# Performance work log

Hardware: AMD Instinct MI355X
Metric: run time of the kernel (lower is better)

Reference implementation:

```python
import jax, jax.numpy as jnp
import numpy as np

D_MODEL, D_STATE, L = 512, 64, 1024
BATCH = 8


def setup_inputs() -> dict:
    key = jax.random.key(0)
    ks = jax.random.split(key, 8)
    dt_min, dt_max = 1e-3, 1e-1
    log_dt = jax.random.uniform(ks[0], (D_MODEL,)) * (np.log(dt_max) - np.log(dt_min)) + np.log(dt_min)
    log_A_real = jnp.log(0.5 * jnp.ones((D_MODEL, D_STATE)))
    A_imag = jnp.pi * jnp.tile(jnp.arange(D_STATE, dtype=jnp.float32), (D_MODEL, 1))
    B_real = jnp.ones((D_MODEL, D_STATE), jnp.float32)
    B_imag = jnp.zeros((D_MODEL, D_STATE), jnp.float32)
    C_real = jax.random.normal(ks[1], (D_MODEL, D_STATE))
    C_imag = jax.random.normal(ks[2], (D_MODEL, D_STATE))
    D = jax.random.normal(ks[3], (D_MODEL,))
    # 1x1 conv (Conv1d kernel_size=1) -> weight (2H, H), bias (2H,)
    conv_w = jax.random.normal(ks[4], (2 * D_MODEL, D_MODEL)) / np.sqrt(D_MODEL)
    conv_b = jnp.zeros((2 * D_MODEL,), jnp.float32)
    dec_w = jax.random.normal(ks[5], (1, D_MODEL)) / np.sqrt(D_MODEL)
    dec_b = jnp.zeros((1,), jnp.float32)
    u = jax.random.normal(ks[6], (BATCH, D_MODEL, L))
    return dict(u=u, log_dt=log_dt, log_A_real=log_A_real, A_imag=A_imag,
                B_real=B_real, B_imag=B_imag, C_real=C_real, C_imag=C_imag,
                D=D, conv_w=conv_w, conv_b=conv_b, dec_w=dec_w, dec_b=dec_b)


def _s4d_kernel(log_dt, log_A_real, A_imag, B_real, B_imag, C_real, C_imag, Lk):
    dt = jnp.exp(log_dt)                              # (H,)
    A = -jnp.exp(log_A_real) + 1j * A_imag            # (H, N) complex
    dtA = A * dt[:, None]                             # (H, N)
    A_bar = jnp.exp(dtA)
    Bc = B_real + 1j * B_imag
    B_bar = (A_bar - 1.0) / A * Bc                    # ZOH discretization
    Cc = C_real + 1j * C_imag
    t = jnp.arange(Lk)                                # (L,)
    # A_bar^t = exp(dtA * t); fuse C*B_bar weighting, reduce over state N
    A_pow = jnp.exp(dtA[:, :, None] * t)              # (H, N, L)
    K = jnp.einsum('hn,hnl->hl', Cc * B_bar, A_pow)   # (H, L) complex
    return K.real


def reference(u, log_dt, log_A_real, A_imag, B_real, B_imag, C_real, C_imag,
              D, conv_w, conv_b, dec_w, dec_b):
    H, Lk = u.shape[1], u.shape[2]
    K = _s4d_kernel(log_dt, log_A_real, A_imag, B_real, B_imag, C_real, C_imag, Lk)
    # depthwise cross-correlation (torch conv1d semantics), padding L-1, keep first L
    y = jax.lax.conv_general_dilated(
        u, K[:, None, :], window_strides=(1,), padding=[(Lk - 1, Lk - 1)],
        feature_group_count=H, dimension_numbers=('NCH', 'OIH', 'NCH'))
    y = y[:, :, :Lk]
    y = y + u * D[:, None]
    y = jax.nn.gelu(y, approximate=False)
    # 1x1 conv + GLU over channel dim
    z = jnp.einsum('oc,bcl->bol', conv_w, y) + conv_b[:, None]
    a, b = jnp.split(z, 2, axis=1)
    y = a * jax.nn.sigmoid(b)                         # (B, H, L)
    pooled = y.mean(axis=-1)                          # (B, H)
    return pooled @ dec_w.T + dec_b                   # (B, 1)
```

## Files before the change

### kernel.cpp

```cpp
#include <hip/hip_runtime.h>
#include <hip/hip_bf16.h>
#include <math.h>

typedef __attribute__((ext_vector_type(8))) short short8;
typedef __attribute__((ext_vector_type(4))) float f32x4;
typedef __attribute__((ext_vector_type(16))) float f32x16;
typedef __attribute__((ext_vector_type(4))) unsigned int uint4v;

constexpr int Hm = 512, Lm = 1024, Bm = 8;

static __device__ __forceinline__ unsigned short f2bf(float f) {
    __hip_bfloat16 h = __float2bfloat16(f);
    return *reinterpret_cast<unsigned short*>(&h);
}
static __device__ __forceinline__ float bf2f(unsigned short u) {
    return __uint_as_float((unsigned)u << 16);
}
static __device__ __forceinline__ uint2 pack4(const unsigned short* x) {
    return make_uint2((unsigned)x[0] | ((unsigned)x[1] << 16),
                      (unsigned)x[2] | ((unsigned)x[3] << 16));
}
static __device__ __forceinline__ short8 ld16u(const char* p) {
    uint2 a = *(const uint2*)p;
    uint2 b = *(const uint2*)(p + 8);
    uint4v t = { a.x, a.y, b.x, b.y };
    return __builtin_bit_cast(short8, t);
}

__global__ __launch_bounds__(256, 2) void k_tconv(const float* __restrict__ log_dt,
                                                  const float* __restrict__ log_A_real,
                                                  const float* __restrict__ A_imag,
                                                  const float* __restrict__ B_real,
                                                  const float* __restrict__ B_imag,
                                                  const float* __restrict__ C_real,
                                                  const float* __restrict__ C_imag,
                                                  const float* __restrict__ conv_w,
                                                  const float* __restrict__ u,
                                                  const float* __restrict__ Dvec,
                                                  unsigned short* __restrict__ Woh,
                                                  unsigned short* __restrict__ YbfH) {
    __shared__ __align__(16) char smem[41984];
    const int tid = threadIdx.x, lane = tid & 63, w = tid >> 6;
    const int h = blockIdx.x;
    const int m = lane & 31, q = lane >> 5;
    const int cg = (lane >> 3) & 3, b = lane & 7;
    float* Kf = (float*)(smem + 36352);
    float* pl = (float*)(smem + 40448);

    float4 ureg[8];
    {
        const int b2 = tid >> 5, t32 = tid & 31;
        const float* ub = u + ((size_t)(b2 * 512 + h)) * 1024;
        #pragma unroll
        for (int g = 0; g < 8; ++g) ureg[g] = *(const float4*)&ub[t32 * 4 + g * 128];
    }
    const float Dh = Dvec[h];

    {
        int i = h * 1024 + tid * 4;
        float4 v = *(const float4*)&conv_w[i];
        *(uint2*)&Woh[i] = make_uint2((unsigned)f2bf(v.x) | ((unsigned)f2bf(v.y) << 16),
                                      (unsigned)f2bf(v.z) | ((unsigned)f2bf(v.w) << 16));
    }
    if (tid < 64) {
        int idx = h * 64 + tid;
        double dt = exp((double)log_dt[h]);
        double Ar = -exp((double)log_A_real[idx]);
        double Ai = (double)A_imag[idx];
        double ar = Ar * dt, ai = Ai * dt;
        double er = exp(ar);
        double rr = er * cos(ai), ri = er * sin(ai);
        double nr = rr - 1.0, ni = ri;
        double den = Ar * Ar + Ai * Ai;
        double qr = (nr * Ar + ni * Ai) / den;
        double qi = (ni * Ar - nr * Ai) / den;
        double Br = (double)B_real[idx], Bi = (double)B_imag[idx];
        double bbr = qr * Br - qi * Bi, bbi = qr * Bi + qi * Br;
        double Cr = (double)C_real[idx], Ci = (double)C_imag[idx];
        double wr = Cr * bbr - Ci * bbi, wi = Cr * bbi + Ci * bbr;
        double e64 = exp(ar * 64.0);
        double p64 = ai * 64.0;
        pl[0 * 64 + tid] = (float)rr;
        pl[1 * 64 + tid] = (float)ri;
        pl[2 * 64 + tid] = (float)wr;
        pl[3 * 64 + tid] = (float)wi;
        pl[4 * 64 + tid] = (float)(e64 * cos(p64));
        pl[5 * 64 + tid] = (float)(e64 * sin(p64));
    }
    __syncthreads();

    {
        float* kl = (float*)(smem + 17792) + w * 1056;
        const float rrf = pl[0 * 64 + lane], rif = pl[1 * 64 + lane];
        float pr = pl[2 * 64 + lane], pi = pl[3 * 64 + lane];
        float br = pl[4 * 64 + lane], bi = pl[5 * 64 + lane];
        int cc = w * 4;
        while (cc) {
            if (cc & 1) { float t_ = pr * br - pi * bi; pi = fmaf(pr, bi, pi * br); pr = t_; }
            float t2 = br * br - bi * bi; bi = 2.f * br * bi; br = t2;
            cc >>= 1;
        }
        const int jj = lane & 15, nq = lane >> 4;
        for (int qq = 0; qq < 16; ++qq) {
            #pragma unroll
            for (int j = 0; j < 16; ++j) {
                kl[j * 66 + lane] = pr;
                float t_ = pr * rrf - pi * rif; pi = fmaf(pr, rif, pi * rrf); pr = t_;
            }
            asm volatile("s_waitcnt lgkmcnt(0)" ::: "memory");
            float s0 = 0.f, s1 = 0.f;
            #pragma unroll
            for (int n = 0; n < 16; n += 4) {
                float2 a = *(const float2*)&kl[jj * 66 + nq * 16 + n];
                float2 b2 = *(const float2*)&kl[jj * 66 + nq * 16 + n + 2];
                s0 += a.x + a.y; s1 += b2.x + b2.y;
            }
            float s = s0 + s1;
            s += __shfl_xor(s, 16);
            s += __shfl_xor(s, 32);
            if (lane < 16) Kf[w * 256 + qq * 16 + jj] = s;
            asm volatile("s_waitcnt lgkmcnt(0)" ::: "memory");
        }
    }
    __syncthreads();

    {
        unsigned int* Gd = (unsigned int*)smem;
        for (int t = tid; t < 4448; t += 256) {
            int s = t / 556;
            int d = t - s * 556;
            int idx0 = 2 * d + s;
            float k0 = (idx0 < 1024) ? Kf[idx0] : 0.f;
            float k1 = (idx0 + 1 < 1024) ? Kf[idx0 + 1] : 0.f;
            Gd[t] = (unsigned)f2bf(k0) | ((unsigned)f2bf(k1) << 16);
        }
    }
    if (tid < 8) { uint4 z = {0, 0, 0, 0}; ((uint4*)(smem + 36224))[tid] = z; }
    __syncthreads();

    {
        const int b2 = tid >> 5, t32 = tid & 31;
        #pragma unroll
        for (int g = 0; g < 8; ++g) {
            int s = t32 * 4 + g * 128;
            float4 v = ureg[g];
            unsigned short t0 = f2bf(v.x), t1 = f2bf(v.y), t2 = f2bf(v.z), t3 = f2bf(v.w);
            int jc = s >> 6, e = s & 63;
            *(uint2*)(smem + 17792 + jc * 1152 + b2 * 144 + e * 2) =
                make_uint2((unsigned)t0 | ((unsigned)t1 << 16),
                           (unsigned)t2 | ((unsigned)t3 << 16));
        }
    }
    __syncthreads();

    const int icg = (cg == 0) ? w : (cg == 1) ? 7 - w : (cg == 2) ? 8 + w : 15 - w;
    const int dmax = 15 - w;

    int aU = 17792 + icg * 1152 + b * 144 + q * 16;
    const int zl = 36224 + q * 16;

    const int sA = (7 - m) & 7;
    int baseH = sA * 2224 + (991 - m - sA + 8 * q) * 2;

    const f32x16 zacc = {};
    f32x16 acc0 = zacc, acc1 = zacc;

    short8 m2, m1, w0, w1, w2, w3;
#define LDA() { const char* pH = smem + baseH; \
        m2 = *(const short8*)(pH +   0); m1 = *(const short8*)(pH +  32); \
        w0 = *(const short8*)(pH +  64); w1 = *(const short8*)(pH +  96); \
        w2 = *(const short8*)(pH + 128); w3 = *(const short8*)(pH + 160); }
    LDA();

    for (int d = 0; d <= dmax; ++d) {
        const char* pb = smem + ((d <= icg) ? aU : zl);
        short8 b0 = *(const short8*)(pb +  0);
        short8 b1 = *(const short8*)(pb + 32);
        short8 b2 = *(const short8*)(pb + 64);
        short8 b3 = *(const short8*)(pb + 96);
        acc0 = __builtin_amdgcn_mfma_f32_32x32x16_bf16(w0, b0, acc0, 0, 0, 0);
        acc1 = __builtin_amdgcn_mfma_f32_32x32x16_bf16(m2, b0, acc1, 0, 0, 0);
        acc0 = __builtin_amdgcn_mfma_f32_32x32x16_bf16(w1, b1, acc0, 0, 0, 0);
        acc1 = __builtin_amdgcn_mfma_f32_32x32x16_bf16(m1, b1, acc1, 0, 0, 0);
        acc0 = __builtin_amdgcn_mfma_f32_32x32x16_bf16(w2, b2, acc0, 0, 0, 0);
        acc1 = __builtin_amdgcn_mfma_f32_32x32x16_bf16(w0, b2, acc1, 0, 0, 0);
        acc0 = __builtin_amdgcn_mfma_f32_32x32x16_bf16(w3, b3, acc0, 0, 0, 0);
        acc1 = __builtin_amdgcn_mfma_f32_32x32x16_bf16(w1, b3, acc1, 0, 0, 0);
        baseH -= 128; aU -= 1152;
        if (d < dmax) LDA();
    }
#undef LDA

    __syncthreads();

    #pragma unroll
    for (int mf = 0; mf < 2; ++mf) {
        const f32x16 ac = mf ? acc1 : acc0;
        #pragma unroll
        for (int rq = 0; rq < 4; ++rq) {
            const int row0 = mf * 32 + 8 * rq + 4 * q;
            uint2 uv2 = *(const uint2*)(smem + 17792 + icg * 1152 + b * 144 + row0 * 2);
            unsigned short us[4] = { (unsigned short)(uv2.x & 0xffff),
                                     (unsigned short)(uv2.x >> 16),
                                     (unsigned short)(uv2.y & 0xffff),
                                     (unsigned short)(uv2.y >> 16) };
            unsigned short oh[4];
            #pragma unroll
            for (int k = 0; k < 4; ++k) {
                float y = ac[rq * 4 + k] + Dh * bf2f(us[k]);
                float g = 0.5f * y * (1.0f + erff(y * 0.70710678118654752f));
                oh[k] = f2bf(g);
            }
            *(uint2*)(smem + icg * 1088 + b * 136 + row0 * 2) = pack4(oh);
        }
    }
    __syncthreads();
    {
        const int b2 = tid >> 5, t32 = tid & 31;
        unsigned short* dst = YbfH + ((size_t)(b2 * 512 + h)) * 1024;
        #pragma unroll
        for (int g = 0; g < 8; ++g) {
            int s = t32 * 4 + g * 128;
            int jc = s >> 6, e = s & 63;
            uint2 v = *(const uint2*)(smem + jc * 1088 + b2 * 136 + e * 2);
            *(uint2*)&dst[s] = v;
        }
    }
}

__global__ __launch_bounds__(256) void k2_gemm(const unsigned short* __restrict__ WbfH,
                                               const unsigned short* __restrict__ Ybf,
                                               const float* __restrict__ conv_b,
                                               const float* __restrict__ dec_w,
                                               float* __restrict__ partial) {
    __shared__ unsigned short WTh[128][40];
    __shared__ unsigned short YT[128][44];
    __shared__ float red[4][64][20];
    const int tid = threadIdx.x, lane = tid & 63, wid = tid >> 6;
    const int b = blockIdx.z, oblk = blockIdx.y, lblk = blockIdx.x;
    const int o0 = oblk * 64, l0 = lblk * 128;
    const int fr = lane & 15, fq = lane >> 4;

    f32x4 acc[8][2] = {};

    const int srow = tid >> 1, skh = (tid & 1) * 16;
    const int grow = (srow < 64) ? (o0 + srow) : (512 + o0 + srow - 64);
    const size_t woff = (size_t)grow * 512 + skh;
    const int cp = tid & 15, lg = tid >> 4;
    const unsigned short* ysb = Ybf + ((size_t)(b * 512 + 2 * cp)) * 1024 + l0 + lg * 8;

    uint4 wc0 = *(const uint4*)(WbfH + woff);
    uint4 wc1 = *(const uint4*)(WbfH + woff + 8);
    uint4 yc0 = *(const uint4*)(ysb);
    uint4 yc1 = *(const uint4*)(ysb + 1024);

    for (int c0 = 0; c0 < 512; c0 += 32) {
        __syncthreads();
        *(uint4*)&WTh[srow][skh]     = wc0;
        *(uint4*)&WTh[srow][skh + 8] = wc1;
        {
            const unsigned int* a = (const unsigned int*)&yc0;
            const unsigned int* c = (const unsigned int*)&yc1;
            #pragma unroll
            for (int t2 = 0; t2 < 4; ++t2) {
                unsigned int lo = (a[t2] & 0xffffu) | (c[t2] << 16);
                unsigned int hi = (a[t2] >> 16) | (c[t2] & 0xffff0000u);
                *(unsigned int*)&YT[lg * 8 + 2 * t2][2 * cp] = lo;
                *(unsigned int*)&YT[lg * 8 + 2 * t2 + 1][2 * cp] = hi;
            }
        }
        if (c0 + 32 < 512) {
            wc0 = *(const uint4*)(WbfH + woff + c0 + 32);
            wc1 = *(const uint4*)(WbfH + woff + c0 + 40);
            const unsigned short* ysn = ysb + (size_t)(c0 + 32) * 1024;
            yc0 = *(const uint4*)(ysn);
            yc1 = *(const uint4*)(ysn + 1024);
        }
        __syncthreads();
        short8 b0h = ld16u((const char*)&YT[wid * 32 + fr][fq * 8]);
        short8 b1h = ld16u((const char*)&YT[wid * 32 + 16 + fr][fq * 8]);
        #pragma unroll
        for (int mf = 0; mf < 8; ++mf) {
            short8 ah = *(const short8*)&WTh[mf * 16 + fr][fq * 8];
            acc[mf][0] = __builtin_amdgcn_mfma_f32_16x16x32_bf16(ah, b0h, acc[mf][0], 0, 0, 0);
            acc[mf][1] = __builtin_amdgcn_mfma_f32_16x16x32_bf16(ah, b1h, acc[mf][1], 0, 0, 0);
        }
    }

    #pragma unroll
    for (int mf = 0; mf < 4; ++mf)
        #pragma unroll
        for (int j = 0; j < 4; ++j) {
            int ol = mf * 16 + fq * 4 + j;
            float ba = conv_b[o0 + ol];
            float bb = conv_b[512 + o0 + ol];
            float s = 0.f;
            #pragma unroll
            for (int nf = 0; nf < 2; ++nf) {
                float za = acc[mf][nf][j] + ba;
                float zb = acc[mf + 4][nf][j] + bb;
                s += za / (1.f + expf(-zb));
            }
            red[wid][ol][fr] = s;
        }
    __syncthreads();
    if (tid < 64) {
        float s = 0.f;
        #pragma unroll
        for (int w = 0; w < 4; ++w) {
            float4 r0 = *(const float4*)&red[w][tid][0];
            float4 r1 = *(const float4*)&red[w][tid][4];
            float4 r2 = *(const float4*)&red[w][tid][8];
            float4 r3 = *(const float4*)&red[w][tid][12];
            s += (r0.x + r0.y + r0.z + r0.w) + (r1.x + r1.y + r1.z + r1.w)
               + (r2.x + r2.y + r2.z + r2.w) + (r3.x + r3.y + r3.z + r3.w);
        }
        float val = s * dec_w[o0 + tid] * (1.0f / 1024.0f);
        #pragma unroll
        for (int off = 32; off; off >>= 1) val += __shfl_xor(val, off);
        if (tid == 0) partial[((b * 8) + oblk) * 8 + lblk] = val;
    }
}

__global__ void k3_final(const float* __restrict__ partial,
                         const float* __restrict__ dec_b,
                         float* __restrict__ out) {
    int b = threadIdx.x;
    if (b < Bm) {
        float s = dec_b[0];
        for (int i = 0; i < 64; ++i) s += partial[b * 64 + i];
        out[b] = s;
    }
}

extern "C" void kernel_launch(void* const* d_in, const int* in_sizes, int n_in,
                              void* d_out, int out_size, void* d_ws, size_t ws_size,
                              hipStream_t stream) {
    const float* u          = (const float*)d_in[0];
    const float* log_dt     = (const float*)d_in[1];
    const float* log_A_real = (const float*)d_in[2];
    const float* A_imag     = (const float*)d_in[3];
    const float* B_real     = (const float*)d_in[4];
    const float* B_imag     = (const float*)d_in[5];
    const float* C_real     = (const float*)d_in[6];
    const float* C_imag     = (const float*)d_in[7];
    const float* Dvec       = (const float*)d_in[8];
    const float* conv_w     = (const float*)d_in[9];
    const float* conv_b     = (const float*)d_in[10];
    const float* dec_w      = (const float*)d_in[11];
    const float* dec_b      = (const float*)d_in[12];

    char* base = (char*)d_ws;
    unsigned short* YbfH = (unsigned short*)base;
    unsigned short* Wh   = (unsigned short*)(base + 8388608);
    float* partial       = (float*)(base + 9437184);
    float* out           = (float*)d_out;

    k_tconv<<<512, 256, 0, stream>>>(log_dt, log_A_real, A_imag, B_real, B_imag,
                                     C_real, C_imag, conv_w, u, Dvec, Wh, YbfH);
    k2_gemm<<<dim3(8, 8, 8), 256, 0, stream>>>(Wh, YbfH, conv_b, dec_w, partial);
    k3_final<<<1, 64, 0, stream>>>(partial, dec_b, out);
}
```

Baseline: 54.90 us.

## Fold final reduction into GEMM via atomic last-block counter and remap blocks

Removes the third kernel launch by having the last GEMM block, found through an atomic counter that the conv kernel resets, sum the partials and write the output. The GEMM grid becomes 1D with a swizzled block-to-tile mapping, likely to change which tiles share cache as blocks are scheduled. One barrier in the conv kernel is also dropped by merging the zero-fill with the bf16 staging of u. This saves a launch and a barrier at the cost of a threadfence and an atomic per block.

```diff
diff --git a/kernel.cpp b/kernel.cpp
--- a/kernel.cpp
+++ b/kernel.cpp
@@ -38,7 +38,8 @@
                                                   const float* __restrict__ u,
                                                   const float* __restrict__ Dvec,
                                                   unsigned short* __restrict__ Woh,
-                                                  unsigned short* __restrict__ YbfH) {
+                                                  unsigned short* __restrict__ YbfH,
+                                                  unsigned int* __restrict__ counter) {
     __shared__ __align__(16) char smem[41984];
     const int tid = threadIdx.x, lane = tid & 63, w = tid >> 6;
     const int h = blockIdx.x;
@@ -46,6 +47,8 @@
     const int cg = (lane >> 3) & 3, b = lane & 7;
     float* Kf = (float*)(smem + 36352);
     float* pl = (float*)(smem + 40448);
+
+    if (h == 0 && tid == 0) *counter = 0;
 
     float4 ureg[8];
     {
@@ -134,11 +137,7 @@
             float k1 = (idx0 + 1 < 1024) ? Kf[idx0 + 1] : 0.f;
             Gd[t] = (unsigned)f2bf(k0) | ((unsigned)f2bf(k1) << 16);
         }
-    }
-    if (tid < 8) { uint4 z = {0, 0, 0, 0}; ((uint4*)(smem + 36224))[tid] = z; }
-    __syncthreads();
-
-    {
+        if (tid < 8) { uint4 z = {0, 0, 0, 0}; ((uint4*)(smem + 36224))[tid] = z; }
         const int b2 = tid >> 5, t32 = tid & 31;
         #pragma unroll
         for (int g = 0; g < 8; ++g) {
@@ -232,12 +231,19 @@
                                                const unsigned short* __restrict__ Ybf,
                                                const float* __restrict__ conv_b,
                                                const float* __restrict__ dec_w,
-                                               float* __restrict__ partial) {
+                                               const float* __restrict__ dec_b,
+                                               float* __restrict__ partial,
+                                               unsigned int* __restrict__ counter,
+                                               float* __restrict__ out) {
     __shared__ unsigned short WTh[128][40];
     __shared__ unsigned short YT[128][44];
     __shared__ float red[4][64][20];
+    __shared__ int last_flag;
     const int tid = threadIdx.x, lane = tid & 63, wid = tid >> 6;
-    const int b = blockIdx.z, oblk = blockIdx.y, lblk = blockIdx.x;
+    const int bid = blockIdx.x;
+    const int wsz = (bid & 7) * 64 + (bid >> 3);
+    const int oblk = wsz & 7, pp = wsz >> 3;
+    const int lblk = pp & 7, b = pp >> 3;
     const int o0 = oblk * 64, l0 = lblk * 128;
     const int fr = lane & 15, fq = lane >> 4;
 
@@ -318,18 +324,20 @@
         float val = s * dec_w[o0 + tid] * (1.0f / 1024.0f);
         #pragma unroll
         for (int off = 32; off; off >>= 1) val += __shfl_xor(val, off);
-        if (tid == 0) partial[((b * 8) + oblk) * 8 + lblk] = val;
-    }
-}
-
-__global__ void k3_final(const float* __restrict__ partial,
-                         const float* __restrict__ dec_b,
-                         float* __restrict__ out) {
-    int b = threadIdx.x;
-    if (b < Bm) {
+        if (tid == 0) {
+            partial[((b * 8) + oblk) * 8 + lblk] = val;
+            __threadfence();
+            unsigned int prev = atomicAdd(counter, 1u);
+            last_flag = (prev == 511u) ? 1 : 0;
+        }
+    }
+    __syncthreads();
+    if (last_flag && tid < 8) {
+        __threadfence();
+        volatile const float* vp = partial;
         float s = dec_b[0];
-        for (int i = 0; i < 64; ++i) s += partial[b * 64 + i];
-        out[b] = s;
+        for (int i = 0; i < 64; ++i) s += vp[tid * 64 + i];
+        out[tid] = s;
     }
 }
 
@@ -351,13 +359,15 @@
     const float* dec_b      = (const float*)d_in[12];
 
     char* base = (char*)d_ws;
-    unsigned short* YbfH = (unsigned short*)base;
-    unsigned short* Wh   = (unsigned short*)(base + 8388608);
-    float* partial       = (float*)(base + 9437184);
-    float* out           = (float*)d_out;
+    unsigned short* YbfH  = (unsigned short*)base;
+    unsigned short* Wh    = (unsigned short*)(base + 8388608);
+    float* partial        = (float*)(base + 9437184);
+    unsigned int* counter = (unsigned int*)(base + 9439232);
+    float* out            = (float*)d_out;
 
     k_tconv<<<512, 256, 0, stream>>>(log_dt, log_A_real, A_imag, B_real, B_imag,
-                                     C_real, C_imag, conv_w, u, Dvec, Wh, YbfH);
-    k2_gemm<<<dim3(8, 8, 8), 256, 0, stream>>>(Wh, YbfH, conv_b, dec_w, partial);
-    k3_final<<<1, 64, 0, stream>>>(partial, dec_b, out);
-}
+                                     C_real, C_imag, conv_w, u, Dvec, Wh, YbfH,
+                                     counter);
+    k2_gemm<<<512, 256, 0, stream>>>(Wh, YbfH, conv_b, dec_w, dec_b,
+                                     partial, counter, out);
+}
```

Result: slower. 69.82 us (+27.2%).
